# Performance work log

Measured on AMD Instinct MI355X. Metric: run time of the kernel, lower is better.

The kernel has to match this reference:

```python
import jax, jax.numpy as jnp
import numpy as np

D = 64      # size_in
RANK = 4    # rank
N = 262144  # batch of samples


def setup_inputs() -> dict:
    key = jax.random.key(0)
    k1, k2, k3, k4, k5 = jax.random.split(key, 5)
    s1 = 1.0 / np.sqrt(D)        # torch Linear init bound for linear1 (in=D)
    s2 = 1.0 / np.sqrt(2 * D)    # bound for linear2 (in=2D)
    return {
        "t": jnp.zeros((1,), dtype=jnp.float32),
        "input_": jax.random.normal(k1, (N, 2 * D), dtype=jnp.float32),
        "W1": jax.random.uniform(k2, (2 * D, D), jnp.float32, -s1, s1),
        "b1": jax.random.uniform(k3, (2 * D,), jnp.float32, -s1, s1),
        "W2": jax.random.uniform(k4, (RANK * D, 2 * D), jnp.float32, -s2, s2),
        "b2": jax.random.uniform(k5, (RANK * D,), jnp.float32, -s2, s2),
    }


def reference(t, input_, W1, b1, W2, b2):
    # Per-sample scalar Hamiltonian H(inp) = sum_j (v . W[:, j])^2 where
    # W = tanh(linear2(tanh(linear1(x)))).reshape(D, RANK); the torch einsum
    # 'mij,mhj,mi,mh->m' factors as sum_j (sum_i W[i,j] v[i])^2.
    def H(inp):
        x, v = inp[:D], inp[D:]
        h = jnp.tanh(W1 @ x + b1)                       # [2D]
        Wm = jnp.tanh(W2 @ h + b2).reshape(D, RANK)     # [D, RANK]
        return jnp.sum((v @ Wm) ** 2)

    # batch_jacobian of a scalar-per-sample fn == per-sample gradient [N, 2D]
    g = jax.vmap(jax.grad(H))(input_)
    dx = g[:, :D]
    dv = -g[:, D:]
    return jnp.concatenate([dx, dv], axis=-1)
```

## Files before the change

kernel.cpp:

```cpp
#include <hip/hip_runtime.h>

#define DD    64
#define TWOD  128
#define RD    256
#define NT    3

typedef __attribute__((ext_vector_type(8))) short short8;
typedef __attribute__((ext_vector_type(4))) float float4v;
typedef __attribute__((ext_vector_type(4))) unsigned uint4v;
typedef unsigned long long ull;
typedef unsigned short ush;

__device__ __forceinline__ ush f2b(float f) {
    unsigned u = __builtin_bit_cast(unsigned, f);
    u += 0x7fffu + ((u >> 16) & 1u);
    return (ush)(u >> 16);
}
__device__ __forceinline__ float b2f(ush s) {
    unsigned u = ((unsigned)s) << 16;
    return __builtin_bit_cast(float, u);
}
__device__ __forceinline__ unsigned cvt_pk_bf16(float lo, float hi) {
    unsigned r;
    asm("v_cvt_pk_bf16_f32 %0, %1, %2" : "=v"(r) : "v"(lo), "v"(hi));
    return r;
}
__device__ __forceinline__ void store_pair(ush* p0, ush* p1, float lo, float hi) {
    unsigned pk = cvt_pk_bf16(lo, hi);
    *p0 = (ush)pk;
    *p1 = (ush)(pk >> 16);
}
__device__ __forceinline__ float ftanh(float x) {
    float e, r;
    asm("v_exp_f32 %0, %1" : "=v"(e) : "v"(x * 2.885390082f));
    asm("v_rcp_f32 %0, %1" : "=v"(r) : "v"(e + 1.0f));
    return __builtin_fmaf(-2.0f, r, 1.0f);
}
__device__ __forceinline__ void lds_fence() {
    asm volatile("s_waitcnt lgkmcnt(0)" ::: "memory");
}

__global__ void prep_weights(const float* __restrict__ W1, const float* __restrict__ W2,
                             ush* __restrict__ wa, ush* __restrict__ wd,
                             ush* __restrict__ wb, ush* __restrict__ wc) {
    int t = blockIdx.x * blockDim.x + threadIdx.x;
    if (t < 8192) {
        wa[t] = f2b(W1[t]);
        int c = t >> 7, r = t & 127;
        wd[t] = f2b(W1[r * 64 + c]);
    }
    if (t < 32768) {
        wb[t] = f2b(W2[t]);
        int c = t >> 8, k = t & 255;
        wc[t] = f2b(W2[k * 128 + c]);
    }
}

__global__ __launch_bounds__(64, 2) void geognn_kernel(
    const float* __restrict__ inp, const float* __restrict__ b1, const float* __restrict__ b2,
    const ush* __restrict__ wa, const ush* __restrict__ wd,
    const ush* __restrict__ wb, const ush* __restrict__ wc,
    float* __restrict__ out, long nrows) {

    __shared__ __align__(16) ush hd_s[NT][16 * 264];
    __shared__ ush v_s[NT][16][68];
    __shared__ float4v y_s[NT][16];

    const int  l   = threadIdx.x;
    const int  l15 = l & 15;
    const int  q   = l >> 4;
    long row0 = (long)blockIdx.x * (16 * NT);
    if (row0 + 16 * NT > nrows) row0 = nrows - 16 * NT;

#pragma unroll
    for (int t = 0; t < NT; ++t)
#pragma unroll
        for (int r = 0; r < 16; r += 2) {
            float v0 = inp[(row0 + t * 16 + r)     * TWOD + DD + l];
            float v1 = inp[(row0 + t * 16 + r + 1) * TWOD + DD + l];
            store_pair(&v_s[t][r][l], &v_s[t][r + 1][l], v0, v1);
        }

    short8 ax[NT][2];
#pragma unroll
    for (int t = 0; t < NT; ++t)
#pragma unroll
        for (int kb = 0; kb < 2; ++kb) {
            const float4v* p = (const float4v*)(inp + (row0 + t * 16 + l15) * TWOD + kb * 32 + q * 8);
            float4v f0 = p[0], f1 = p[1];
            uint4v pk = { cvt_pk_bf16(f0.x, f0.y), cvt_pk_bf16(f0.z, f0.w),
                          cvt_pk_bf16(f1.x, f1.y), cvt_pk_bf16(f1.z, f1.w) };
            ax[t][kb] = __builtin_bit_cast(short8, pk);
        }

    float b1v[8];
#pragma unroll
    for (int nb = 0; nb < 8; ++nb) b1v[nb] = b1[nb * 16 + l15];
    float b2v[16];
#pragma unroll
    for (int nb = 0; nb < 16; ++nb) b2v[nb] = b2[nb * 16 + l15];

    short8 aw[16];
#pragma unroll
    for (int h = 0; h < 16; ++h)
        aw[h] = *(const short8*)(wa + ((h >> 1) * 16 + l15) * DD + (h & 1) * 32 + q * 8);

    unsigned g1p[NT][16];
#pragma unroll
    for (int nb = 0; nb < 8; ++nb) {
        const int c = nb * 16 + l15;
#pragma unroll
        for (int t = 0; t < NT; ++t) {
            float4v acc = {0.f, 0.f, 0.f, 0.f};
            acc = __builtin_amdgcn_mfma_f32_16x16x32_bf16(ax[t][0], aw[nb * 2 + 0], acc, 0, 0, 0);
            acc = __builtin_amdgcn_mfma_f32_16x16x32_bf16(ax[t][1], aw[nb * 2 + 1], acc, 0, 0, 0);
#pragma unroll
            for (int i = 0; i < 4; i += 2) {
                float h0 = ftanh(acc[i]     + b1v[nb]);
                float h1 = ftanh(acc[i + 1] + b1v[nb]);
                store_pair(&hd_s[t][(q * 4 + i) * 136 + c],
                           &hd_s[t][(q * 4 + i + 1) * 136 + c], h0, h1);
                g1p[t][nb * 2 + (i >> 1)] = cvt_pk_bf16(1.f - h0 * h0, 1.f - h1 * h1);
            }
        }
    }

    short8 bwA[8], bwB[8];
#pragma unroll
    for (int h = 0; h < 8; ++h)
        bwA[h] = *(const short8*)(wb + ((h >> 2) * 16 + l15) * TWOD + (h & 3) * 32 + q * 8);

    lds_fence();

    short8 ha[NT][4];
#pragma unroll
    for (int t = 0; t < NT; ++t)
#pragma unroll
        for (int kb = 0; kb < 4; ++kb)
            ha[t][kb] = *(const short8*)(&hd_s[t][l15 * 136 + kb * 32 + q * 8]);

    lds_fence();

    float yp[NT][4] = {};
#pragma unroll
    for (int p = 0; p < 8; ++p) {
        short8* cur = (p & 1) ? bwB : bwA;
        short8* nxt = (p & 1) ? bwA : bwB;
        if (p < 7) {
#pragma unroll
            for (int h = 0; h < 8; ++h)
                nxt[h] = *(const short8*)(wb + (((p + 1) * 2 + (h >> 2)) * 16 + l15) * TWOD
                                          + (h & 3) * 32 + q * 8);
        }
#pragma unroll
        for (int s = 0; s < 2; ++s) {
            const int nb = p * 2 + s;
            const int n  = nb * 16 + l15;
            const int c4 = nb * 4 + (l15 >> 2);
#pragma unroll
            for (int t = 0; t < NT; ++t) {
                float4v acc = {0.f, 0.f, 0.f, 0.f};
#pragma unroll
                for (int kb = 0; kb < 4; ++kb)
                    acc = __builtin_amdgcn_mfma_f32_16x16x32_bf16(ha[t][kb], cur[s * 4 + kb], acc, 0, 0, 0);
                float u0 = ftanh(acc[0] + b2v[nb]);
                float u1 = ftanh(acc[1] + b2v[nb]);
                float u2 = ftanh(acc[2] + b2v[nb]);
                float u3 = ftanh(acc[3] + b2v[nb]);
                store_pair(&hd_s[t][(q * 4 + 0) * 264 + n], &hd_s[t][(q * 4 + 1) * 264 + n], u0, u1);
                store_pair(&hd_s[t][(q * 4 + 2) * 264 + n], &hd_s[t][(q * 4 + 3) * 264 + n], u2, u3);
                yp[t][0] += b2f(v_s[t][q * 4 + 0][c4]) * u0;
                yp[t][1] += b2f(v_s[t][q * 4 + 1][c4]) * u1;
                yp[t][2] += b2f(v_s[t][q * 4 + 2][c4]) * u2;
                yp[t][3] += b2f(v_s[t][q * 4 + 3][c4]) * u3;
            }
        }
    }

#pragma unroll
    for (int t = 0; t < NT; ++t)
#pragma unroll
        for (int i = 0; i < 4; ++i) {
            yp[t][i] += __shfl_xor(yp[t][i], 4, 64);
            yp[t][i] += __shfl_xor(yp[t][i], 8, 64);
        }
    if (l15 < 4) {
#pragma unroll
        for (int t = 0; t < NT; ++t)
#pragma unroll
            for (int i = 0; i < 4; ++i)
                ((float*)&y_s[t][q * 4 + i])[l15] = yp[t][i];
    }

    short8 cwA[8], cwB[8];
#pragma unroll
    for (int kb = 0; kb < 8; ++kb)
        cwA[kb] = *(const short8*)(wc + l15 * RD + kb * 32 + q * 8);

    lds_fence();

#pragma unroll
    for (int t = 0; t < NT; ++t)
#pragma unroll
        for (int r = 0; r < 16; ++r) {
            ull uu = *(const ull*)(&hd_s[t][r * 264 + 4 * l]);
            float4v y = y_s[t][r];
            float vv = b2f(v_s[t][r][l]);
            float u0 = b2f((ush)uu);
            float u1 = b2f((ush)(uu >> 16));
            float u2 = b2f((ush)(uu >> 32));
            float u3 = b2f((ush)(uu >> 48));
            float dvv = y.x * u0 + y.y * u1 + y.z * u2 + y.w * u3;
            out[(row0 + t * 16 + r) * TWOD + DD + l] = -2.0f * dvv;
            float t0 = 2.0f * y.x * vv * (1.0f - u0 * u0);
            float t1 = 2.0f * y.y * vv * (1.0f - u1 * u1);
            float t2 = 2.0f * y.z * vv * (1.0f - u2 * u2);
            float t3 = 2.0f * y.w * vv * (1.0f - u3 * u3);
            unsigned w0 = cvt_pk_bf16(t0, t1);
            unsigned w1 = cvt_pk_bf16(t2, t3);
            ull w = (ull)w0 | ((ull)w1 << 32);
            *(ull*)(&hd_s[t][r * 264 + 4 * l]) = w;
        }

    lds_fence();

    short8 da[NT][8];
#pragma unroll
    for (int t = 0; t < NT; ++t)
#pragma unroll
        for (int kb = 0; kb < 8; ++kb)
            da[t][kb] = *(const short8*)(&hd_s[t][l15 * 264 + kb * 32 + q * 8]);

    lds_fence();

#pragma unroll
    for (int nb = 0; nb < 8; ++nb) {
        short8* cur = (nb & 1) ? cwB : cwA;
        short8* nxt = (nb & 1) ? cwA : cwB;
        if (nb < 7) {
#pragma unroll
            for (int kb = 0; kb < 8; ++kb)
                nxt[kb] = *(const short8*)(wc + ((nb + 1) * 16 + l15) * RD + kb * 32 + q * 8);
        }
        const int c = nb * 16 + l15;
#pragma unroll
        for (int t = 0; t < NT; ++t) {
            float4v acc = {0.f, 0.f, 0.f, 0.f};
#pragma unroll
            for (int kb = 0; kb < 8; ++kb)
                acc = __builtin_amdgcn_mfma_f32_16x16x32_bf16(da[t][kb], cur[kb], acc, 0, 0, 0);
            unsigned glo = g1p[t][nb * 2 + 0], ghi = g1p[t][nb * 2 + 1];
            float d0 = acc[0] * b2f((ush)glo);
            float d1 = acc[1] * b2f((ush)(glo >> 16));
            float d2 = acc[2] * b2f((ush)ghi);
            float d3 = acc[3] * b2f((ush)(ghi >> 16));
            store_pair(&hd_s[t][(q * 4 + 0) * 136 + c], &hd_s[t][(q * 4 + 1) * 136 + c], d0, d1);
            store_pair(&hd_s[t][(q * 4 + 2) * 136 + c], &hd_s[t][(q * 4 + 3) * 136 + c], d2, d3);
        }
    }

    short8 dw[16];
#pragma unroll
    for (int h = 0; h < 16; ++h)
        dw[h] = *(const short8*)(wd + ((h >> 2) * 16 + l15) * TWOD + (h & 3) * 32 + q * 8);

    lds_fence();

    short8 dfa[NT][4];
#pragma unroll
    for (int t = 0; t < NT; ++t)
#pragma unroll
        for (int kb = 0; kb < 4; ++kb)
            dfa[t][kb] = *(const short8*)(&hd_s[t][l15 * 136 + kb * 32 + q * 8]);
#pragma unroll
    for (int t = 0; t < NT; ++t)
#pragma unroll
        for (int nb = 0; nb < 4; ++nb) {
            float4v acc = {0.f, 0.f, 0.f, 0.f};
#pragma unroll
            for (int kb = 0; kb < 4; ++kb)
                acc = __builtin_amdgcn_mfma_f32_16x16x32_bf16(dfa[t][kb], dw[nb * 4 + kb], acc, 0, 0, 0);
#pragma unroll
            for (int i = 0; i < 4; ++i)
                out[(row0 + t * 16 + q * 4 + i) * TWOD + nb * 16 + l15] = acc[i];
        }
}

extern "C" void kernel_launch(void* const* d_in, const int* in_sizes, int n_in,
                              void* d_out, int out_size, void* d_ws, size_t ws_size,
                              hipStream_t stream) {
    const float* inp = (const float*)d_in[1];
    const float* W1  = (const float*)d_in[2];
    const float* b1  = (const float*)d_in[3];
    const float* W2  = (const float*)d_in[4];
    const float* b2  = (const float*)d_in[5];

    ush* wa = (ush*)d_ws;
    ush* wd = wa + 8192;
    ush* wb = wd + 8192;
    ush* wc = wb + 32768;

    prep_weights<<<128, 256, 0, stream>>>(W1, W2, wa, wd, wb, wc);

    const long rows = in_sizes[1] / TWOD;
    const int  grid = (int)((rows + 16 * NT - 1) / (16 * NT));
    geognn_kernel<<<grid, 64, 0, stream>>>(inp, b1, b2, wa, wd, wb, wc,
                                           (float*)d_out, rows);
}
```

Before: 345.8 us.

## Drop explicit LDS waitcnt fences, add nontemporal IO, setprio around MFMA, lazy bias loads

Replaces the explicit s_waitcnt lgkmcnt(0) fences with compiler-only memory barriers, so the compiler inserts its own waits and can overlap LDS traffic. Input loads and output stores become nontemporal to reduce cache pollution. Wave priority is raised around the MFMA chains, and bias values are loaded inside the loops instead of being held in registers up front, to ease register pressure. Each wave works on its own LDS region, so correctness relies on the compiler's automatic waitcnt insertion.

Measured after the change: 366.6 us. 1.06x slower.

```diff
diff --git a/kernel.cpp b/kernel.cpp
--- a/kernel.cpp
+++ b/kernel.cpp
@@ -36,8 +36,8 @@
     asm("v_rcp_f32 %0, %1" : "=v"(r) : "v"(e + 1.0f));
     return __builtin_fmaf(-2.0f, r, 1.0f);
 }
-__device__ __forceinline__ void lds_fence() {
-    asm volatile("s_waitcnt lgkmcnt(0)" ::: "memory");
+__device__ __forceinline__ void phase_fence() {
+    asm volatile("" ::: "memory");
 }
 
 __global__ void prep_weights(const float* __restrict__ W1, const float* __restrict__ W2,
@@ -76,8 +76,8 @@
     for (int t = 0; t < NT; ++t)
 #pragma unroll
         for (int r = 0; r < 16; r += 2) {
-            float v0 = inp[(row0 + t * 16 + r)     * TWOD + DD + l];
-            float v1 = inp[(row0 + t * 16 + r + 1) * TWOD + DD + l];
+            float v0 = __builtin_nontemporal_load(&inp[(row0 + t * 16 + r)     * TWOD + DD + l]);
+            float v1 = __builtin_nontemporal_load(&inp[(row0 + t * 16 + r + 1) * TWOD + DD + l]);
             store_pair(&v_s[t][r][l], &v_s[t][r + 1][l], v0, v1);
         }
 
@@ -87,19 +87,13 @@
 #pragma unroll
         for (int kb = 0; kb < 2; ++kb) {
             const float4v* p = (const float4v*)(inp + (row0 + t * 16 + l15) * TWOD + kb * 32 + q * 8);
-            float4v f0 = p[0], f1 = p[1];
+            float4v f0 = __builtin_nontemporal_load(p);
+            float4v f1 = __builtin_nontemporal_load(p + 1);
             uint4v pk = { cvt_pk_bf16(f0.x, f0.y), cvt_pk_bf16(f0.z, f0.w),
                           cvt_pk_bf16(f1.x, f1.y), cvt_pk_bf16(f1.z, f1.w) };
             ax[t][kb] = __builtin_bit_cast(short8, pk);
         }
 
-    float b1v[8];
-#pragma unroll
-    for (int nb = 0; nb < 8; ++nb) b1v[nb] = b1[nb * 16 + l15];
-    float b2v[16];
-#pragma unroll
-    for (int nb = 0; nb < 16; ++nb) b2v[nb] = b2[nb * 16 + l15];
-
     short8 aw[16];
 #pragma unroll
     for (int h = 0; h < 16; ++h)
@@ -108,6 +102,7 @@
     unsigned g1p[NT][16];
 #pragma unroll
     for (int nb = 0; nb < 8; ++nb) {
+        float bv = b1[nb * 16 + l15];
         const int c = nb * 16 + l15;
 #pragma unroll
         for (int t = 0; t < NT; ++t) {
@@ -116,8 +111,8 @@
             acc = __builtin_amdgcn_mfma_f32_16x16x32_bf16(ax[t][1], aw[nb * 2 + 1], acc, 0, 0, 0);
 #pragma unroll
             for (int i = 0; i < 4; i += 2) {
-                float h0 = ftanh(acc[i]     + b1v[nb]);
-                float h1 = ftanh(acc[i + 1] + b1v[nb]);
+                float h0 = ftanh(acc[i]     + bv);
+                float h1 = ftanh(acc[i + 1] + bv);
                 store_pair(&hd_s[t][(q * 4 + i) * 136 + c],
                            &hd_s[t][(q * 4 + i + 1) * 136 + c], h0, h1);
                 g1p[t][nb * 2 + (i >> 1)] = cvt_pk_bf16(1.f - h0 * h0, 1.f - h1 * h1);
@@ -130,7 +125,7 @@
     for (int h = 0; h < 8; ++h)
         bwA[h] = *(const short8*)(wb + ((h >> 2) * 16 + l15) * TWOD + (h & 3) * 32 + q * 8);
 
-    lds_fence();
+    phase_fence();
 
     short8 ha[NT][4];
 #pragma unroll
@@ -139,7 +134,7 @@
         for (int kb = 0; kb < 4; ++kb)
             ha[t][kb] = *(const short8*)(&hd_s[t][l15 * 136 + kb * 32 + q * 8]);
 
-    lds_fence();
+    phase_fence();
 
     float yp[NT][4] = {};
 #pragma unroll
@@ -157,16 +152,19 @@
             const int nb = p * 2 + s;
             const int n  = nb * 16 + l15;
             const int c4 = nb * 4 + (l15 >> 2);
+            float bv = b2[nb * 16 + l15];
 #pragma unroll
             for (int t = 0; t < NT; ++t) {
                 float4v acc = {0.f, 0.f, 0.f, 0.f};
+                __builtin_amdgcn_s_setprio(1);
 #pragma unroll
                 for (int kb = 0; kb < 4; ++kb)
                     acc = __builtin_amdgcn_mfma_f32_16x16x32_bf16(ha[t][kb], cur[s * 4 + kb], acc, 0, 0, 0);
-                float u0 = ftanh(acc[0] + b2v[nb]);
-                float u1 = ftanh(acc[1] + b2v[nb]);
-                float u2 = ftanh(acc[2] + b2v[nb]);
-                float u3 = ftanh(acc[3] + b2v[nb]);
+                __builtin_amdgcn_s_setprio(0);
+                float u0 = ftanh(acc[0] + bv);
+                float u1 = ftanh(acc[1] + bv);
+                float u2 = ftanh(acc[2] + bv);
+                float u3 = ftanh(acc[3] + bv);
                 store_pair(&hd_s[t][(q * 4 + 0) * 264 + n], &hd_s[t][(q * 4 + 1) * 264 + n], u0, u1);
                 store_pair(&hd_s[t][(q * 4 + 2) * 264 + n], &hd_s[t][(q * 4 + 3) * 264 + n], u2, u3);
                 yp[t][0] += b2f(v_s[t][q * 4 + 0][c4]) * u0;
@@ -197,7 +195,7 @@
     for (int kb = 0; kb < 8; ++kb)
         cwA[kb] = *(const short8*)(wc + l15 * RD + kb * 32 + q * 8);
 
-    lds_fence();
+    phase_fence();
 
 #pragma unroll
     for (int t = 0; t < NT; ++t)
@@ -211,7 +209,7 @@
             float u2 = b2f((ush)(uu >> 32));
             float u3 = b2f((ush)(uu >> 48));
             float dvv = y.x * u0 + y.y * u1 + y.z * u2 + y.w * u3;
-            out[(row0 + t * 16 + r) * TWOD + DD + l] = -2.0f * dvv;
+            __builtin_nontemporal_store(-2.0f * dvv, &out[(row0 + t * 16 + r) * TWOD + DD + l]);
             float t0 = 2.0f * y.x * vv * (1.0f - u0 * u0);
             float t1 = 2.0f * y.y * vv * (1.0f - u1 * u1);
             float t2 = 2.0f * y.z * vv * (1.0f - u2 * u2);
@@ -222,7 +220,7 @@
             *(ull*)(&hd_s[t][r * 264 + 4 * l]) = w;
         }
 
-    lds_fence();
+    phase_fence();
 
     short8 da[NT][8];
 #pragma unroll
@@ -231,7 +229,7 @@
         for (int kb = 0; kb < 8; ++kb)
             da[t][kb] = *(const short8*)(&hd_s[t][l15 * 264 + kb * 32 + q * 8]);
 
-    lds_fence();
+    phase_fence();
 
 #pragma unroll
     for (int nb = 0; nb < 8; ++nb) {
@@ -246,9 +244,11 @@
 #pragma unroll
         for (int t = 0; t < NT; ++t) {
             float4v acc = {0.f, 0.f, 0.f, 0.f};
+            __builtin_amdgcn_s_setprio(1);
 #pragma unroll
             for (int kb = 0; kb < 8; ++kb)
                 acc = __builtin_amdgcn_mfma_f32_16x16x32_bf16(da[t][kb], cur[kb], acc, 0, 0, 0);
+            __builtin_amdgcn_s_setprio(0);
             unsigned glo = g1p[t][nb * 2 + 0], ghi = g1p[t][nb * 2 + 1];
             float d0 = acc[0] * b2f((ush)glo);
             float d1 = acc[1] * b2f((ush)(glo >> 16));
@@ -264,7 +264,7 @@
     for (int h = 0; h < 16; ++h)
         dw[h] = *(const short8*)(wd + ((h >> 2) * 16 + l15) * TWOD + (h & 3) * 32 + q * 8);
 
-    lds_fence();
+    phase_fence();
 
     short8 dfa[NT][4];
 #pragma unroll
@@ -282,7 +282,8 @@
                 acc = __builtin_amdgcn_mfma_f32_16x16x32_bf16(dfa[t][kb], dw[nb * 4 + kb], acc, 0, 0, 0);
 #pragma unroll
             for (int i = 0; i < 4; ++i)
-                out[(row0 + t * 16 + q * 4 + i) * TWOD + nb * 16 + l15] = acc[i];
+                __builtin_nontemporal_store(acc[i],
+                    &out[(row0 + t * 16 + q * 4 + i) * TWOD + nb * 16 + l15]);
         }
 }
 
```
